# Kernel tuning notes

Measured on AMD Instinct MI355X. Metric: run time of the kernel, lower is better.

## Reference

```python
import jax, jax.numpy as jnp
import numpy as np

T, B, IN, H, OUT = 1024, 128, 6, 1536, 5


def setup_inputs() -> dict:
    key = jax.random.key(0)
    ks = jax.random.split(key, 11)
    s = 1.0 / np.sqrt(H)  # PyTorch cell init range
    u = lambda k, shape: jax.random.uniform(k, shape, jnp.float32, -s, s)
    return {
        "rnn_input": jax.random.normal(ks[0], (T, B, IN), jnp.float32),
        "W_ih0": u(ks[1], (4 * H, IN)),
        "W_hh0": u(ks[2], (4 * H, H)),
        "b_ih0": u(ks[3], (4 * H,)),
        "b_hh0": u(ks[4], (4 * H,)),
        "W_ih1": u(ks[5], (4 * H, H)),
        "W_hh1": u(ks[6], (4 * H, H)),
        "b_ih1": u(ks[7], (4 * H,)),
        "b_hh1": u(ks[8], (4 * H,)),
        "W_lin": u(ks[9], (OUT, H)),
        "b_lin": u(ks[10], (OUT,)),
    }


def _lstm_cell(x, h, c, W_ih, W_hh, b):
    # PyTorch LSTMCell: gates ordered (input, forget, cell, output)
    gates = x @ W_ih.T + h @ W_hh.T + b  # [B, 4H]
    i, f, g, o = jnp.split(gates, 4, axis=-1)
    c_new = jax.nn.sigmoid(f) * c + jax.nn.sigmoid(i) * jnp.tanh(g)
    h_new = jax.nn.sigmoid(o) * jnp.tanh(c_new)
    return h_new, c_new


def reference(rnn_input, W_ih0, W_hh0, b_ih0, b_hh0,
              W_ih1, W_hh1, b_ih1, b_hh1, W_lin, b_lin):
    b0 = b_ih0 + b_hh0
    b1 = b_ih1 + b_hh1
    batch = rnn_input.shape[1]
    h = rnn_input.dtype
    z = jnp.zeros((batch, H), h)

    def step(carry, x_t):
        h0, c0, h1, c1 = carry
        h0, c0 = _lstm_cell(x_t, h0, c0, W_ih0, W_hh0, b0)
        h1, c1 = _lstm_cell(h0, h1, c1, W_ih1, W_hh1, b1)
        return (h0, c0, h1, c1), None

    (h0, c0, h1, c1), _ = jax.lax.scan(step, (z, z, z, z), rnn_input)
    # Module's forward returns only the last-timestep linear output
    return h1 @ W_lin.T + b_lin  # [B, OUT]
```

## Files before the change

kernel.cpp:

```cpp
#include <hip/hip_runtime.h>

#define TSTEPS 1024
#define BATCH  128
#define HDIM   1536
#define NBLK   224
#define NB_L0  96
#define K0P    1600
#define K1P    3072

typedef _Float16 f16x8 __attribute__((ext_vector_type(8)));
typedef float    f32x4 __attribute__((ext_vector_type(4)));

#define OFF_H0   256ul
#define OFF_H1   (OFF_H0 + 2ul*BATCH*HDIM*2)
#define OFF_WP0  (OFF_H1 + 2ul*BATCH*HDIM*2)
#define OFF_WP1  (OFF_WP0 + 96ul*64*K0P*2)
#define OFF_WLP  (OFF_WP1 + 128ul*48*K1P*2)
#define WS_NEED  (OFF_WLP + 16ul*HDIM*2)

#define SM_PARK  98304
#define SM_CST   147456
#define SM_BG    155648
#define SM_BYTES 155904

#define MFMA(a,b,c) __builtin_amdgcn_mfma_f32_16x16x32_f16(a,b,c,0,0,0)
#define LDSBAR()  asm volatile("s_waitcnt lgkmcnt(0)\n\ts_barrier" ::: "memory")
#define WAITVM8() asm volatile("s_waitcnt vmcnt(8)" ::: "memory")
#define WAITVM0() asm volatile("s_waitcnt vmcnt(0)" ::: "memory")

__device__ __forceinline__ float sgf(float x) { return 1.f/(1.f + __expf(-x)); }
__device__ __forceinline__ float thf(float x) { float e = __expf(2.f*x); return 1.f - 2.f/(e+1.f); }

__device__ __forceinline__ void gld16(const _Float16* g, char* lds) {
  __builtin_amdgcn_global_load_lds(
      (const __attribute__((address_space(1))) unsigned int*)g,
      (__attribute__((address_space(3))) unsigned int*)lds, 16, 0, 0);
}

__device__ __forceinline__ void grid_bar(unsigned* cnt, unsigned target) {
  __syncthreads();
  if (threadIdx.x == 0) {
    __hip_atomic_fetch_add(cnt, 1u, __ATOMIC_RELEASE, __HIP_MEMORY_SCOPE_AGENT);
    while (__hip_atomic_load(cnt, __ATOMIC_RELAXED, __HIP_MEMORY_SCOPE_AGENT) < target)
      __builtin_amdgcn_s_sleep(2);
    __builtin_amdgcn_fence(__ATOMIC_ACQUIRE, "agent");
  }
  __syncthreads();
}

__global__ void convert_weights(const float* __restrict__ Wih0, const float* __restrict__ Whh0,
                                const float* __restrict__ Wih1, const float* __restrict__ Whh1,
                                const float* __restrict__ Wlin,
                                _Float16* __restrict__ Wp0, _Float16* __restrict__ Wp1,
                                _Float16* __restrict__ Wlp) {
  const unsigned N0 = 96u*64u*K0P, N1 = 128u*48u*K1P, N2 = 16u*HDIM;
  const unsigned NT = N0 + N1 + N2;
  for (unsigned i = blockIdx.x*blockDim.x + threadIdx.x; i < NT; i += gridDim.x*blockDim.x) {
    if (i < N0) {
      unsigned blk = i / (64u*K0P), r = i - blk*64u*K0P;
      unsigned p = r / K0P, kk = r - p*K0P;
      unsigned srow = (p>>4)*HDIM + blk*16 + (p&15);
      float v;
      if (kk < 64u) v = (kk < 6u) ? Wih0[srow*6 + kk] : 0.f;
      else          v = Whh0[(size_t)srow*HDIM + (kk-64u)];
      Wp0[i] = (_Float16)v;
    } else if (i < N0 + N1) {
      unsigned ii = i - N0;
      unsigned blk = ii / (48u*K1P), r = ii - blk*48u*K1P;
      unsigned p = r / K1P, kk = r - p*K1P;
      unsigned srow = (p/12u)*HDIM + blk*12 + (p%12u);
      float v = (kk < (unsigned)HDIM) ? Wih1[(size_t)srow*HDIM + kk]
                                      : Whh1[(size_t)srow*HDIM + (kk-HDIM)];
      Wp1[ii] = (_Float16)v;
    } else {
      unsigned ii = i - N0 - N1;
      unsigned rr = ii / HDIM, k = ii - rr*HDIM;
      Wlp[ii] = (_Float16)(rr < 5 ? Wlin[rr*HDIM + k] : 0.f);
    }
  }
}

__global__ __launch_bounds__(256, 1) void lstm_persistent(
    const float* __restrict__ xall,
    const float* __restrict__ bih0, const float* __restrict__ bhh0,
    const float* __restrict__ bih1, const float* __restrict__ bhh1,
    const float* __restrict__ blin,
    const _Float16* __restrict__ Wp0, const _Float16* __restrict__ Wp1,
    const _Float16* __restrict__ Wlp,
    _Float16* __restrict__ h0b, _Float16* __restrict__ h1b,
    unsigned* __restrict__ cnt, float* __restrict__ out)
{
  extern __shared__ __align__(16) char smem[];
  char*  park = smem + SM_PARK;
  float* cst  = (float*)(smem + SM_CST);
  float* bg   = (float*)(smem + SM_BG);
  float* gbuf = (float*)smem;

  const int tid = threadIdx.x, bid = blockIdx.x;
  const int wv = tid >> 6, lane = tid & 63, q = lane >> 4, l15 = lane & 15;
  const int BH = BATCH*HDIM;
  unsigned barc = 0;

  int dmaoff[8];
#pragma unroll
  for (int i = 0; i < 8; ++i) {
    int m = wv*32 + i*4 + (lane>>4), w16 = lane & 15;
    int u = (w16 & 8) | ((w16 ^ (m & 7)) & 7);
    dmaoff[i] = m*HDIM + u*8;
  }
  const int uA = wv*4 + q;
  int addrA[8];
#pragma unroll
  for (int mt = 0; mt < 8; ++mt) {
    int m = mt*16 + l15;
    int swz = (uA & 8) | ((uA ^ (m & 7)) & 7);
    addrA[mt] = m*256 + swz*16;
  }

  if (bid < NB_L0) {
    for (int p = tid; p < 64; p += 256) {
      int srow = (p>>4)*HDIM + (bid<<4) + (p&15);
      bg[p] = bih0[srow] + bhh0[srow];
    }
    for (int i = tid; i < BATCH*16; i += 256) cst[i] = 0.f;
    f16x8 bw[13][4];
#pragma unroll
    for (int wi = 0; wi < 13; ++wi)
#pragma unroll
      for (int nt = 0; nt < 4; ++nt)
        bw[wi][nt] = *(const f16x8*)(Wp0 + ((size_t)(bid*64 + nt*16 + l15))*K0P
                                         + (4*wi + wv)*32 + q*8);
    __syncthreads();

#pragma unroll 1
    for (int s = 0; s < TSTEPS; ++s) {
      const _Float16* h0r = h0b + ((s+1)&1)*BH;
      _Float16*       h0w = h0b + (s&1)*BH;
      const float*    xs  = xall + (size_t)s*BATCH*6;

#pragma unroll
      for (int i = 0; i < 8; ++i)
        gld16(h0r + 64 + dmaoff[i], smem + 32768 + (wv*8+i)*1024);
#pragma unroll
      for (int i = 0; i < 4; ++i) {
        int sidx = i*256 + tid, m = sidx>>3, w8 = sidx&7;
        int u = w8 ^ (m & 7);
        f16x8 v = {0,0,0,0,0,0,0,0};
        if (u == 0) {
#pragma unroll
          for (int j = 0; j < 6; ++j) v[j] = (_Float16)xs[m*6 + j];
        }
        *(f16x8*)(smem + m*256 + w8*16) = v;
      }
#pragma unroll
      for (int i = 0; i < 4; ++i) {
        int sidx = i*256 + tid, m = sidx>>3, w8 = sidx&7;
        int u8 = (w8 ^ (m & 7)) & 7;
        f16x8 hv = *(const f16x8*)(h0r + m*HDIM + u8*8);
        *(f16x8*)(smem + m*256 + (8 + w8)*16) = hv;
      }
      f32x4 acc[8][4];
#pragma unroll
      for (int mt = 0; mt < 8; ++mt)
#pragma unroll
        for (int nt = 0; nt < 4; ++nt) { f32x4 z = {0,0,0,0}; acc[mt][nt] = z; }

#pragma unroll
      for (int wi = 0; wi < 13; ++wi) {
        if (wi == 12)      WAITVM0();
        else if (wi >= 1)  WAITVM8();
        LDSBAR();
        if (wi + 2 < 13) {
          const _Float16* src = h0r + (wi+2)*128 - 64;
          char* dst = smem + ((wi+2)%3)*32768;
#pragma unroll
          for (int i = 0; i < 8; ++i) gld16(src + dmaoff[i], dst + (wv*8+i)*1024);
        }
        if (4*wi + wv < 50) {
          const char* bs = smem + (wi%3)*32768;
#pragma unroll
          for (int mt = 0; mt < 8; ++mt) {
            f16x8 a = *(const f16x8*)(bs + addrA[mt]);
#pragma unroll
            for (int nt = 0; nt < 4; ++nt)
              acc[mt][nt] = MFMA(a, bw[wi][nt], acc[mt][nt]);
          }
        }
      }
      LDSBAR();

#pragma unroll
      for (int r = 0; r < 4; ++r) {
        int nt = (wv + r) & 3;
#pragma unroll
        for (int mt = 0; mt < 8; ++mt) {
          f32x4 av = (nt==0)?acc[mt][0]:(nt==1)?acc[mt][1]:(nt==2)?acc[mt][2]:acc[mt][3];
          float* p = gbuf + (nt*16 + l15)*132 + (mt*16 + q*4);
          if (r == 0) *(f32x4*)p = av;
          else        { f32x4 o = *(const f32x4*)p; *(f32x4*)p = o + av; }
        }
        LDSBAR();
      }
#pragma unroll
      for (int e = 0; e < 8; ++e) {
        int idx = e*256 + tid, m = idx>>4, j = idx&15;
        float gi = gbuf[j*132 + m]        + bg[j];
        float gf = gbuf[(16+j)*132 + m]   + bg[16+j];
        float gg = gbuf[(32+j)*132 + m]   + bg[32+j];
        float go = gbuf[(48+j)*132 + m]   + bg[48+j];
        float co = cst[m*16 + j];
        float cn = sgf(gf)*co + sgf(gi)*thf(gg);
        cst[m*16 + j] = cn;
        h0w[(size_t)m*HDIM + (bid<<4) + j] = (_Float16)(sgf(go)*thf(cn));
      }
      barc += NBLK; grid_bar(cnt, barc);
    }
    barc += NBLK; grid_bar(cnt, barc);
  } else {
    const int bid1 = bid - NB_L0;
    for (int p = tid; p < 48; p += 256) {
      int srow = (p/12)*HDIM + bid1*12 + (p%12);
      bg[p] = bih1[srow] + bhh1[srow];
    }
    for (int i = tid; i < 64*12; i += 256) cst[i] = 0.f;
    f16x8 bw1[20][3];
#pragma unroll
    for (int wi = 0; wi < 20; ++wi)
#pragma unroll
      for (int nt = 0; nt < 3; ++nt)
        bw1[wi][nt] = *(const f16x8*)(Wp1 + ((size_t)(bid1*48 + nt*16 + l15))*K1P
                                          + (4*wi + wv)*32 + q*8);
    for (int idx = tid; idx < 16*3*64; idx += 256) {
      int cl = idx/192, rem = idx - cl*192, nt = rem>>6, l = rem&63;
      f16x8 v = *(const f16x8*)(Wp1 + ((size_t)(bid1*48 + nt*16 + (l&15)))*K1P
                                    + (80 + cl)*32 + (l>>4)*8);
      *(f16x8*)(park + idx*16) = v;
    }
    __syncthreads();
    barc += NBLK; grid_bar(cnt, barc);

#pragma unroll 1
    for (int s = 1; s <= TSTEPS; ++s) {
      const _Float16* h0r = h0b + ((s-1)&1)*BH;
      const _Float16* h1r = h1b + (s&1)*BH;
      _Float16*       h1w = h1b + ((s-1)&1)*BH;

#pragma unroll
      for (int i = 0; i < 8; ++i) gld16(h0r +   0 + dmaoff[i], smem +     0 + (wv*8+i)*1024);
#pragma unroll
      for (int i = 0; i < 8; ++i) gld16(h0r + 128 + dmaoff[i], smem + 32768 + (wv*8+i)*1024);
      f32x4 acc[8][3];
#pragma unroll
      for (int mt = 0; mt < 8; ++mt)
#pragma unroll
        for (int nt = 0; nt < 3; ++nt) { f32x4 z = {0,0,0,0}; acc[mt][nt] = z; }

#pragma unroll
      for (int wi = 0; wi < 24; ++wi) {
        if (wi == 23) WAITVM0(); else WAITVM8();
        LDSBAR();
        if (wi + 2 < 24) {
          int wn = wi + 2;
          const _Float16* src = (wn < 12) ? (h0r + wn*128) : (h1r + (wn-12)*128);
          char* dst = smem + (wn%3)*32768;
#pragma unroll
          for (int i = 0; i < 8; ++i) gld16(src + dmaoff[i], dst + (wv*8+i)*1024);
        }
        const char* bs = smem + (wi%3)*32768;
        if (wi < 20) {
#pragma unroll
          for (int mt = 0; mt < 8; ++mt) {
            f16x8 a = *(const f16x8*)(bs + addrA[mt]);
#pragma unroll
            for (int nt = 0; nt < 3; ++nt)
              acc[mt][nt] = MFMA(a, bw1[wi][nt], acc[mt][nt]);
          }
        } else {
          f16x8 p0 = *(const f16x8*)(park + ((((wi-20)*4 + wv)*3 + 0)*64 + lane)*16);
          f16x8 p1 = *(const f16x8*)(park + ((((wi-20)*4 + wv)*3 + 1)*64 + lane)*16);
          f16x8 p2 = *(const f16x8*)(park + ((((wi-20)*4 + wv)*3 + 2)*64 + lane)*16);
#pragma unroll
          for (int mt = 0; mt < 8; ++mt) {
            f16x8 a = *(const f16x8*)(bs + addrA[mt]);
            acc[mt][0] = MFMA(a, p0, acc[mt][0]);
            acc[mt][1] = MFMA(a, p1, acc[mt][1]);
            acc[mt][2] = MFMA(a, p2, acc[mt][2]);
          }
        }
      }
      LDSBAR();

#pragma unroll
      for (int r = 0; r < 4; ++r) {
        int nt = (wv + r) & 3;
        if (nt < 3) {
#pragma unroll
          for (int mt = 0; mt < 8; ++mt) {
            f32x4 av = (nt==0)?acc[mt][0]:(nt==1)?acc[mt][1]:acc[mt][2];
            float* p = gbuf + (nt*16 + l15)*132 + (mt*16 + q*4);
            if (r == 0 || (r == 1 && wv == 3)) {
            }
            if (r == 0) *(f32x4*)p = av;
            else        { f32x4 o = *(const f32x4*)p; *(f32x4*)p = o + av; }
          }
        }
        LDSBAR();
      }
#pragma unroll
      for (int e = 0; e < 8; ++e) {
        int idx = e*256 + tid, m = idx>>4, j = idx&15;
        if (j < 12) {
          float gi = gbuf[j*132 + m]        + bg[j];
          float gf = gbuf[(12+j)*132 + m]   + bg[12+j];
          float gg = gbuf[(24+j)*132 + m]   + bg[24+j];
          float go = gbuf[(36+j)*132 + m]   + bg[36+j];
          float co = cst[m*12 + j];
          float cn = sgf(gf)*co + sgf(gi)*thf(gg);
          cst[m*12 + j] = cn;
          h1w[(size_t)m*HDIM + bid1*12 + j] = (_Float16)(sgf(go)*thf(cn));
        }
      }
      barc += NBLK; grid_bar(cnt, barc);
    }
  }

  if (bid == 0) {
    const _Float16* h1r = h1b + ((TSTEPS-1)&1)*BH;
    f32x4 a8[8];
#pragma unroll
    for (int i = 0; i < 8; ++i) { f32x4 z = {0,0,0,0}; a8[i] = z; }
    for (int c = wv*12; c < wv*12 + 12; ++c) {
      f16x8 bf = *(const f16x8*)(Wlp + (size_t)l15*HDIM + c*32 + q*8);
#pragma unroll
      for (int mt = 0; mt < 8; ++mt) {
        f16x8 a = *(const f16x8*)(h1r + (size_t)(mt*16 + l15)*HDIM + c*32 + q*8);
        a8[mt] = MFMA(a, bf, a8[mt]);
      }
    }
    float* pl = (float*)smem;
#pragma unroll
    for (int mt = 0; mt < 8; ++mt)
#pragma unroll
      for (int rg = 0; rg < 4; ++rg)
        pl[wv*2048 + (mt*16 + q*4 + rg)*16 + l15] = a8[mt][rg];
    __syncthreads();
    for (int e = tid; e < 640; e += 256) {
      int b = e/5, o = e - 5*b;
      out[e] = blin[o] + pl[b*16+o] + pl[2048 + b*16+o] + pl[4096 + b*16+o] + pl[6144 + b*16+o];
    }
  }
}

extern "C" void kernel_launch(void* const* d_in, const int* in_sizes, int n_in,
                              void* d_out, int out_size, void* d_ws, size_t ws_size,
                              hipStream_t stream) {
  (void)in_sizes; (void)n_in; (void)out_size;
  if (ws_size < WS_NEED) return;

  const float* x    = (const float*)d_in[0];
  const float* Wih0 = (const float*)d_in[1];
  const float* Whh0 = (const float*)d_in[2];
  const float* bih0 = (const float*)d_in[3];
  const float* bhh0 = (const float*)d_in[4];
  const float* Wih1 = (const float*)d_in[5];
  const float* Whh1 = (const float*)d_in[6];
  const float* bih1 = (const float*)d_in[7];
  const float* bhh1 = (const float*)d_in[8];
  const float* Wlin = (const float*)d_in[9];
  const float* blin = (const float*)d_in[10];

  char* ws = (char*)d_ws;
  unsigned*  cnt = (unsigned*)ws;
  _Float16*  h0b = (_Float16*)(ws + OFF_H0);
  _Float16*  h1b = (_Float16*)(ws + OFF_H1);
  _Float16*  Wp0 = (_Float16*)(ws + OFF_WP0);
  _Float16*  Wp1 = (_Float16*)(ws + OFF_WP1);
  _Float16*  Wlp = (_Float16*)(ws + OFF_WLP);
  float*     out = (float*)d_out;

  hipMemsetAsync(ws, 0, OFF_WP0, stream);
  hipLaunchKernelGGL(convert_weights, dim3(4096), dim3(256), 0, stream,
                     Wih0, Whh0, Wih1, Whh1, Wlin, Wp0, Wp1, Wlp);

  hipFuncSetAttribute((const void*)lstm_persistent,
                      hipFuncAttributeMaxDynamicSharedMemorySize, 160*1024);

  void* args[13];
  args[0]  = (void*)&x;    args[1]  = (void*)&bih0; args[2]  = (void*)&bhh0;
  args[3]  = (void*)&bih1; args[4]  = (void*)&bhh1; args[5]  = (void*)&blin;
  args[6]  = (void*)&Wp0;  args[7]  = (void*)&Wp1;  args[8]  = (void*)&Wlp;
  args[9]  = (void*)&h0b;  args[10] = (void*)&h1b;  args[11] = (void*)&cnt;
  args[12] = (void*)&out;
  hipError_t err = hipLaunchCooperativeKernel((const void*)lstm_persistent,
                                              dim3(NBLK), dim3(256),
                                              args, (unsigned)SM_BYTES, stream);
  if (err != hipSuccess) {
    hipLaunchKernelGGL(lstm_persistent, dim3(NBLK), dim3(256), SM_BYTES, stream,
                       x, bih0, bhh0, bih1, bhh1, blin, Wp0, Wp1, Wlp,
                       h0b, h1b, cnt, out);
  }
}
```

Measured before the change: 29.67 ms.

## Replace global grid barrier with per-layer sharded counters and decoupled wavefront

Swaps the single all-block grid barrier for separate layer-0 and layer-1 counters, each split across 8 cache-line-spaced slots, so each layer only synchronizes within its own group. Layer 0 now runs ahead of layer 1 by up to a few steps using a 4-deep h0 ring buffer, waiting on layer 1 only when it would overwrite a still-needed slot. Layer 1 waits just for layer-0 completion of the step it consumes. This is meant to cut barrier cost and let the two layers pipeline, at the cost of more h0 buffer space and more delicate cross-group ordering.

```diff
diff --git a/kernel.cpp b/kernel.cpp
--- a/kernel.cpp
+++ b/kernel.cpp
@@ -3,16 +3,19 @@
 #define TSTEPS 1024
 #define BATCH  128
 #define HDIM   1536
-#define NBLK   224
 #define NB_L0  96
+#define NB_L1  128
+#define NBLK   (NB_L0 + NB_L1)
 #define K0P    1600
 #define K1P    3072
 
 typedef _Float16 f16x8 __attribute__((ext_vector_type(8)));
 typedef float    f32x4 __attribute__((ext_vector_type(4)));
 
-#define OFF_H0   256ul
-#define OFF_H1   (OFF_H0 + 2ul*BATCH*HDIM*2)
+#define OFF_C0   0ul
+#define OFF_C1   1024ul
+#define OFF_H0   4096ul
+#define OFF_H1   (OFF_H0 + 4ul*BATCH*HDIM*2)
 #define OFF_WP0  (OFF_H1 + 2ul*BATCH*HDIM*2)
 #define OFF_WP1  (OFF_WP0 + 96ul*64*K0P*2)
 #define OFF_WLP  (OFF_WP1 + 128ul*48*K1P*2)
@@ -37,12 +40,25 @@
       (__attribute__((address_space(3))) unsigned int*)lds, 16, 0, 0);
 }
 
-__device__ __forceinline__ void grid_bar(unsigned* cnt, unsigned target) {
+__device__ __forceinline__ void group_bar(unsigned* lines, unsigned target, int tid) {
   __syncthreads();
-  if (threadIdx.x == 0) {
-    __hip_atomic_fetch_add(cnt, 1u, __ATOMIC_RELEASE, __HIP_MEMORY_SCOPE_AGENT);
-    while (__hip_atomic_load(cnt, __ATOMIC_RELAXED, __HIP_MEMORY_SCOPE_AGENT) < target)
-      __builtin_amdgcn_s_sleep(2);
+  if (tid == 0)
+    __hip_atomic_fetch_add(lines + (blockIdx.x & 7)*32, 1u,
+                           __ATOMIC_RELEASE, __HIP_MEMORY_SCOPE_AGENT);
+  if (tid < 8) {
+    while (__hip_atomic_load(lines + tid*32, __ATOMIC_RELAXED,
+                             __HIP_MEMORY_SCOPE_AGENT) < target)
+      __builtin_amdgcn_s_sleep(1);
+    __builtin_amdgcn_fence(__ATOMIC_ACQUIRE, "agent");
+  }
+  __syncthreads();
+}
+
+__device__ __forceinline__ void wait_group(unsigned* lines, unsigned target, int tid) {
+  if (tid < 8) {
+    while (__hip_atomic_load(lines + tid*32, __ATOMIC_RELAXED,
+                             __HIP_MEMORY_SCOPE_AGENT) < target)
+      __builtin_amdgcn_s_sleep(1);
     __builtin_amdgcn_fence(__ATOMIC_ACQUIRE, "agent");
   }
   __syncthreads();
@@ -88,7 +104,8 @@
     const _Float16* __restrict__ Wp0, const _Float16* __restrict__ Wp1,
     const _Float16* __restrict__ Wlp,
     _Float16* __restrict__ h0b, _Float16* __restrict__ h1b,
-    unsigned* __restrict__ cnt, float* __restrict__ out)
+    unsigned* __restrict__ c0l, unsigned* __restrict__ c1l,
+    float* __restrict__ out)
 {
   extern __shared__ __align__(16) char smem[];
   char*  park = smem + SM_PARK;
@@ -99,7 +116,6 @@
   const int tid = threadIdx.x, bid = blockIdx.x;
   const int wv = tid >> 6, lane = tid & 63, q = lane >> 4, l15 = lane & 15;
   const int BH = BATCH*HDIM;
-  unsigned barc = 0;
 
   int dmaoff[8];
 #pragma unroll
@@ -134,8 +150,10 @@
 
 #pragma unroll 1
     for (int s = 0; s < TSTEPS; ++s) {
-      const _Float16* h0r = h0b + ((s+1)&1)*BH;
-      _Float16*       h0w = h0b + (s&1)*BH;
+      if (s >= 4) wait_group(c1l, 16u*(unsigned)(s-3), tid);
+
+      const _Float16* h0r = h0b + (size_t)((s+3)&3)*BH;
+      _Float16*       h0w = h0b + (size_t)(s&3)*BH;
       const float*    xs  = xall + (size_t)s*BATCH*6;
 
 #pragma unroll
@@ -213,9 +231,8 @@
         cst[m*16 + j] = cn;
         h0w[(size_t)m*HDIM + (bid<<4) + j] = (_Float16)(sgf(go)*thf(cn));
       }
-      barc += NBLK; grid_bar(cnt, barc);
-    }
-    barc += NBLK; grid_bar(cnt, barc);
+      group_bar(c0l, 12u*(unsigned)(s+1), tid);
+    }
   } else {
     const int bid1 = bid - NB_L0;
     for (int p = tid; p < 48; p += 256) {
@@ -237,13 +254,14 @@
       *(f16x8*)(park + idx*16) = v;
     }
     __syncthreads();
-    barc += NBLK; grid_bar(cnt, barc);
 
 #pragma unroll 1
     for (int s = 1; s <= TSTEPS; ++s) {
-      const _Float16* h0r = h0b + ((s-1)&1)*BH;
-      const _Float16* h1r = h1b + (s&1)*BH;
-      _Float16*       h1w = h1b + ((s-1)&1)*BH;
+      wait_group(c0l, 12u*(unsigned)s, tid);
+
+      const _Float16* h0r = h0b + (size_t)((s-1)&3)*BH;
+      const _Float16* h1r = h1b + (size_t)(s&1)*BH;
+      _Float16*       h1w = h1b + (size_t)((s-1)&1)*BH;
 
 #pragma unroll
       for (int i = 0; i < 8; ++i) gld16(h0r +   0 + dmaoff[i], smem +     0 + (wv*8+i)*1024);
@@ -298,8 +316,6 @@
           for (int mt = 0; mt < 8; ++mt) {
             f32x4 av = (nt==0)?acc[mt][0]:(nt==1)?acc[mt][1]:acc[mt][2];
             float* p = gbuf + (nt*16 + l15)*132 + (mt*16 + q*4);
-            if (r == 0 || (r == 1 && wv == 3)) {
-            }
             if (r == 0) *(f32x4*)p = av;
             else        { f32x4 o = *(const f32x4*)p; *(f32x4*)p = o + av; }
           }
@@ -320,33 +336,33 @@
           h1w[(size_t)m*HDIM + bid1*12 + j] = (_Float16)(sgf(go)*thf(cn));
         }
       }
-      barc += NBLK; grid_bar(cnt, barc);
-    }
-  }
-
-  if (bid == 0) {
-    const _Float16* h1r = h1b + ((TSTEPS-1)&1)*BH;
-    f32x4 a8[8];
-#pragma unroll
-    for (int i = 0; i < 8; ++i) { f32x4 z = {0,0,0,0}; a8[i] = z; }
-    for (int c = wv*12; c < wv*12 + 12; ++c) {
-      f16x8 bf = *(const f16x8*)(Wlp + (size_t)l15*HDIM + c*32 + q*8);
-#pragma unroll
-      for (int mt = 0; mt < 8; ++mt) {
-        f16x8 a = *(const f16x8*)(h1r + (size_t)(mt*16 + l15)*HDIM + c*32 + q*8);
-        a8[mt] = MFMA(a, bf, a8[mt]);
-      }
-    }
-    float* pl = (float*)smem;
-#pragma unroll
-    for (int mt = 0; mt < 8; ++mt)
-#pragma unroll
-      for (int rg = 0; rg < 4; ++rg)
-        pl[wv*2048 + (mt*16 + q*4 + rg)*16 + l15] = a8[mt][rg];
-    __syncthreads();
-    for (int e = tid; e < 640; e += 256) {
-      int b = e/5, o = e - 5*b;
-      out[e] = blin[o] + pl[b*16+o] + pl[2048 + b*16+o] + pl[4096 + b*16+o] + pl[6144 + b*16+o];
+      group_bar(c1l, 16u*(unsigned)s, tid);
+    }
+
+    if (bid == NB_L0) {
+      const _Float16* h1r = h1b + (size_t)((TSTEPS-1)&1)*BH;
+      f32x4 a8[8];
+#pragma unroll
+      for (int i = 0; i < 8; ++i) { f32x4 z = {0,0,0,0}; a8[i] = z; }
+      for (int c = wv*12; c < wv*12 + 12; ++c) {
+        f16x8 bf = *(const f16x8*)(Wlp + (size_t)l15*HDIM + c*32 + q*8);
+#pragma unroll
+        for (int mt = 0; mt < 8; ++mt) {
+          f16x8 a = *(const f16x8*)(h1r + (size_t)(mt*16 + l15)*HDIM + c*32 + q*8);
+          a8[mt] = MFMA(a, bf, a8[mt]);
+        }
+      }
+      float* pl = (float*)smem;
+#pragma unroll
+      for (int mt = 0; mt < 8; ++mt)
+#pragma unroll
+        for (int rg = 0; rg < 4; ++rg)
+          pl[wv*2048 + (mt*16 + q*4 + rg)*16 + l15] = a8[mt][rg];
+      __syncthreads();
+      for (int e = tid; e < 640; e += 256) {
+        int b = e/5, o = e - 5*b;
+        out[e] = blin[o] + pl[b*16+o] + pl[2048 + b*16+o] + pl[4096 + b*16+o] + pl[6144 + b*16+o];
+      }
     }
   }
 }
@@ -370,7 +386,8 @@
   const float* blin = (const float*)d_in[10];
 
   char* ws = (char*)d_ws;
-  unsigned*  cnt = (unsigned*)ws;
+  unsigned*  c0l = (unsigned*)(ws + OFF_C0);
+  unsigned*  c1l = (unsigned*)(ws + OFF_C1);
   _Float16*  h0b = (_Float16*)(ws + OFF_H0);
   _Float16*  h1b = (_Float16*)(ws + OFF_H1);
   _Float16*  Wp0 = (_Float16*)(ws + OFF_WP0);
@@ -385,18 +402,18 @@
   hipFuncSetAttribute((const void*)lstm_persistent,
                       hipFuncAttributeMaxDynamicSharedMemorySize, 160*1024);
 
-  void* args[13];
+  void* args[14];
   args[0]  = (void*)&x;    args[1]  = (void*)&bih0; args[2]  = (void*)&bhh0;
   args[3]  = (void*)&bih1; args[4]  = (void*)&bhh1; args[5]  = (void*)&blin;
   args[6]  = (void*)&Wp0;  args[7]  = (void*)&Wp1;  args[8]  = (void*)&Wlp;
-  args[9]  = (void*)&h0b;  args[10] = (void*)&h1b;  args[11] = (void*)&cnt;
-  args[12] = (void*)&out;
+  args[9]  = (void*)&h0b;  args[10] = (void*)&h1b;  args[11] = (void*)&c0l;
+  args[12] = (void*)&c1l;  args[13] = (void*)&out;
   hipError_t err = hipLaunchCooperativeKernel((const void*)lstm_persistent,
                                               dim3(NBLK), dim3(256),
                                               args, (unsigned)SM_BYTES, stream);
   if (err != hipSuccess) {
     hipLaunchKernelGGL(lstm_persistent, dim3(NBLK), dim3(256), SM_BYTES, stream,
                        x, bih0, bhh0, bih1, bhh1, blin, Wp0, Wp1, Wlp,
-                       h0b, h1b, cnt, out);
-  }
-}
+                       h0b, h1b, c0l, c1l, out);
+  }
+}
```

Result: faster. 28.01 ms (-5.6%).
